# Performance work log

Measured on AMD Instinct MI355X. Metric: run time of the kernel, lower is better.

The kernel has to match this reference:

```python
import jax, jax.numpy as jnp
import numpy as np

B, Q, K, D, H, HD, OUT = 4, 1024, 1024, 256, 8, 32, 256


def setup_inputs() -> dict:
    key = jax.random.key(0)
    ks = jax.random.split(key, 11)
    s = 0.05  # small init scale for weights
    return {
        "q_data": jax.random.normal(ks[0], (B, Q, D), jnp.float32),
        "m_data": jax.random.normal(ks[1], (B, K, D), jnp.float32),
        "bias": jax.random.normal(ks[2], (B, 1, 1, K), jnp.float32),
        "nonbatched_bias": jax.random.normal(ks[3], (H, Q, K), jnp.float32),
        "query_w": jax.random.normal(ks[4], (D, H, HD), jnp.float32) * s,
        "key_w": jax.random.normal(ks[5], (D, H, HD), jnp.float32) * s,
        "value_w": jax.random.normal(ks[6], (D, H, HD), jnp.float32) * s,
        "gating_w": jax.random.normal(ks[7], (D, H, HD), jnp.float32) * s,
        "gating_b": jnp.ones((H, HD), jnp.float32),
        "output_w": jax.random.normal(ks[8], (H, HD, OUT), jnp.float32) * s,
        "output_b": jnp.zeros((OUT,), jnp.float32),
    }


def reference(q_data, m_data, bias, nonbatched_bias, query_w, key_w, value_w,
              gating_w, gating_b, output_w, output_b):
    key_dim = query_w.shape[-1]
    # QKV projections; queries pre-scaled by 1/sqrt(head_dim)
    q = jnp.einsum('bqa,ahc->bqhc', q_data, query_w) * key_dim ** (-0.5)
    k = jnp.einsum('bka,ahc->bkhc', m_data, key_w)
    v = jnp.einsum('bka,ahc->bkhc', m_data, value_w)
    # attention logits [b,h,q,k] plus batched and nonbatched additive biases
    logits_update = jnp.einsum('bqhc,bkhc->bhqk', q, k)
    logits = logits_update + bias + nonbatched_bias[None]
    weights = jax.nn.softmax(logits, axis=-1)
    weighted_avg = jnp.einsum('bhqk,bkhc->bqhc', weights, v)
    # sigmoid gating on the value-aggregated output
    gate = jax.nn.sigmoid(jnp.einsum('bqc,chv->bqhv', q_data, gating_w) + gating_b)
    weighted_avg = weighted_avg * gate
    output = jnp.einsum('bqhc,hco->bqo', weighted_avg, output_w) + output_b
    return (output, logits_update)
```

## Files before the change

kernel.cpp:

```cpp
#include <hip/hip_runtime.h>
#include <hip/hip_bf16.h>

#define NB 4
#define NQ 1024
#define NKS 1024
#define ND 256
#define NH 8
#define NHD 32
#define NOUT 256
#define SPLIT 4

typedef __attribute__((ext_vector_type(8))) short v8s;
typedef __attribute__((ext_vector_type(4))) short v4s;
typedef __attribute__((ext_vector_type(4))) float f32x4;

__global__ __launch_bounds__(256) void prep_all(
    const float* __restrict__ qd, const float* __restrict__ md,
    const float* __restrict__ qw, const float* __restrict__ kw,
    const float* __restrict__ vw, const float* __restrict__ gw,
    const float* __restrict__ ow,
    __hip_bfloat16* __restrict__ Abf, __hip_bfloat16* __restrict__ Wt)
{
  if (blockIdx.x < 1024) {
    const int gid = blockIdx.x * 256 + threadIdx.x;
    const float* src = (gid < 131072) ? qd : md;
    const size_t off = (size_t)(gid & 131071) * 8;
    const float4 a = ((const float4*)(src + off))[0];
    const float4 c = ((const float4*)(src + off))[1];
    __hip_bfloat16 t8[8];
    t8[0]=__float2bfloat16(a.x); t8[1]=__float2bfloat16(a.y);
    t8[2]=__float2bfloat16(a.z); t8[3]=__float2bfloat16(a.w);
    t8[4]=__float2bfloat16(c.x); t8[5]=__float2bfloat16(c.y);
    t8[6]=__float2bfloat16(c.z); t8[7]=__float2bfloat16(c.w);
    *(v8s*)(Abf + (size_t)gid * 8) = *(v8s*)t8;
    return;
  }
  __shared__ float tile[64][65];
  const int wb = blockIdx.x - 1024;
  const int m = wb >> 4, bx = wb & 15;
  const float* src = (m == 0) ? qw : (m == 1) ? kw : (m == 2) ? vw
                   : (m == 3) ? gw : ow;
  const float scale = (m == 0) ? 0.1767766952966369f : 1.0f;
  const int d0 = (bx >> 2) * 64, o0 = (bx & 3) * 64;
  #pragma unroll
  for (int i = 0; i < 16; ++i) {
    const int idx = threadIdx.x + i * 256;
    tile[idx >> 6][idx & 63] = src[(size_t)(d0 + (idx >> 6)) * 256 + o0 + (idx & 63)];
  }
  __syncthreads();
  __hip_bfloat16* dst = Wt + (size_t)m * 65536;
  #pragma unroll
  for (int i = 0; i < 16; ++i) {
    const int idx = threadIdx.x + i * 256;
    const int orow = idx >> 6, dc = idx & 63;
    dst[(size_t)(o0 + orow) * 256 + d0 + dc] = __float2bfloat16(tile[dc][orow] * scale);
  }
}

__global__ __launch_bounds__(256) void proj_kernel(
    const __hip_bfloat16* __restrict__ Abf, const __hip_bfloat16* __restrict__ Wt,
    const float* __restrict__ gating_b,
    __hip_bfloat16* __restrict__ Qw, __hip_bfloat16* __restrict__ Kw,
    __hip_bfloat16* __restrict__ Vt, __hip_bfloat16* __restrict__ G)
{
  const int wv = threadIdx.x >> 6, lane = threadIdx.x & 63;
  const int c = lane & 15, g = lane >> 4;
  const int task = blockIdx.x * 4 + wv;
  const int ctg = task & 3;
  const int mat = (task >> 2) & 1;
  const int r0g = (task >> 3) & 255;
  const int src = task >> 11;
  const int r0 = r0g * 16;
  const int b = r0 >> 10, pos0 = r0 & 1023;
  const f32x4 z = {0.f, 0.f, 0.f, 0.f};

  const __hip_bfloat16* A = Abf + ((size_t)src * 4096 + r0) * 256;
  v8s af[8];
  #pragma unroll
  for (int ks = 0; ks < 8; ++ks)
    af[ks] = *(const v8s*)(A + c * 256 + ks * 32 + g * 8);

  const int widx = (src == 0) ? (mat ? 3 : 0) : (mat ? 2 : 1);
  const __hip_bfloat16* W = Wt + (size_t)widx * 65536;
  const bool swapped = (src == 1) && (mat == 1);

  f32x4 ac[4] = {z, z, z, z};
  #pragma unroll
  for (int ks = 0; ks < 8; ++ks) {
    #pragma unroll
    for (int j = 0; j < 4; ++j) {
      v8s wf = *(const v8s*)(W + (size_t)((ctg * 4 + j) * 16 + c) * 256 + ks * 32 + g * 8);
      ac[j] = swapped
        ? __builtin_amdgcn_mfma_f32_16x16x32_bf16(wf, af[ks], ac[j], 0, 0, 0)
        : __builtin_amdgcn_mfma_f32_16x16x32_bf16(af[ks], wf, ac[j], 0, 0, 0);
    }
  }

  if (src == 0 && mat == 0) {
    #pragma unroll
    for (int j = 0; j < 4; ++j) {
      const int o = (ctg * 4 + j) * 16 + c, h = o >> 5, hd = o & 31;
      #pragma unroll
      for (int r = 0; r < 4; ++r)
        Qw[((size_t)(b * NH + h) * 1024 + pos0 + 4 * g + r) * 32 + hd] =
            __float2bfloat16(ac[j][r]);
    }
  } else if (src == 0) {
    #pragma unroll
    for (int j = 0; j < 4; ++j) {
      const int o = (ctg * 4 + j) * 16 + c;
      const float gb = gating_b[o];
      #pragma unroll
      for (int r = 0; r < 4; ++r)
        G[(size_t)(r0 + 4 * g + r) * 256 + o] = __float2bfloat16(ac[j][r] + gb);
    }
  } else if (mat == 0) {
    #pragma unroll
    for (int j = 0; j < 4; ++j) {
      const int o = (ctg * 4 + j) * 16 + c, h = o >> 5, hd = o & 31;
      #pragma unroll
      for (int r = 0; r < 4; ++r)
        Kw[((size_t)(b * NH + h) * 1024 + pos0 + 4 * g + r) * 32 + hd] =
            __float2bfloat16(ac[j][r]);
    }
  } else {
    #pragma unroll
    for (int j = 0; j < 4; ++j) {
      #pragma unroll
      for (int r = 0; r < 4; ++r) {
        const int o2 = (ctg * 4 + j) * 16 + 4 * g + r;
        Vt[((size_t)(b * NH + (o2 >> 5)) * 32 + (o2 & 31)) * 1024 + pos0 + c] =
            __float2bfloat16(ac[j][r]);
      }
    }
  }
}

__global__ __launch_bounds__(256, 2) void attn_kernel(
    const __hip_bfloat16* __restrict__ Qw, const __hip_bfloat16* __restrict__ Kw,
    const __hip_bfloat16* __restrict__ Vt,
    const float* __restrict__ bias, const float* __restrict__ nbb,
    float* __restrict__ out_logits,
    __hip_bfloat16* __restrict__ partO, float* __restrict__ partL)
{
  __shared__ __align__(16) __hip_bfloat16 sP[4][16][72];

  const int wv = threadIdx.x >> 6, lane = threadIdx.x & 63;
  const int c = lane & 15, g = lane >> 4;
  const int xcd   = blockIdx.x & 7;
  const int slot  = blockIdx.x >> 3;
  const int bh    = ((slot >> 6) << 3) | xcd;
  const int inner = slot & 63;
  const int sp    = inner >> 4;
  const int qtg   = inner & 15;
  const int qt  = qtg * 4 + wv;
  const int b = bh >> 3, h = bh & 7;
  const int rem = bh * 64 + qt;
  const int q0 = qt * 16;
  const int kbase = sp * (NKS / SPLIT);
  const size_t bhs = (size_t)bh;

  const __hip_bfloat16* Kbase = Kw + bhs * NKS * NHD;
  const __hip_bfloat16* Vbase = Vt + bhs * NHD * NKS;
  const float* biasb = bias + (size_t)b * NKS;
  const float* nbbb  = nbb + ((size_t)h * NQ + q0) * NKS;

  const v8s qfrag = *(const v8s*)(Qw + (bhs * NQ + q0 + c) * NHD + g * 8);

  const f32x4 zacc = {0.f, 0.f, 0.f, 0.f};
  f32x4 O0 = zacc, O1 = zacc;
  float lsumL[4] = {0.f, 0.f, 0.f, 0.f};

  auto loadKV = [&](int k0, v8s* kf, v8s* vf) {
    kf[0] = *(const v8s*)(Kbase + (k0 +      c) * NHD + g * 8);
    kf[1] = *(const v8s*)(Kbase + (k0 + 16 + c) * NHD + g * 8);
    kf[2] = *(const v8s*)(Kbase + (k0 + 32 + c) * NHD + g * 8);
    kf[3] = *(const v8s*)(Kbase + (k0 + 48 + c) * NHD + g * 8);
    vf[0] = *(const v8s*)(Vbase + (     c) * NKS + k0 +      g * 8);
    vf[1] = *(const v8s*)(Vbase + (16 + c) * NKS + k0 +      g * 8);
    vf[2] = *(const v8s*)(Vbase + (     c) * NKS + k0 + 32 + g * 8);
    vf[3] = *(const v8s*)(Vbase + (16 + c) * NKS + k0 + 32 + g * 8);
  };
  auto loadBias = [&](int k0, float* bn) {
    #pragma unroll
    for (int t = 0; t < 4; ++t) {
      const float bvt = biasb[k0 + t * 16 + c];
      #pragma unroll
      for (int r = 0; r < 4; ++r)
        bn[t * 4 + r] = bvt + nbbb[(g * 4 + r) * NKS + k0 + t * 16 + c];
    }
  };

  auto compute = [&](int k0, const v8s* kf, const v8s* vf, const float* bn) {
    f32x4 S[4];
    #pragma unroll
    for (int t = 0; t < 4; ++t)
      S[t] = __builtin_amdgcn_mfma_f32_16x16x32_bf16(qfrag, kf[t], zacc, 0, 0, 0);

    #pragma unroll
    for (int r = 0; r < 4; ++r) {
      const int qrow = q0 + g * 4 + r;
      float* lp = out_logits + (bhs * NQ + qrow) * (size_t)NKS + k0 + c;
      float psum = 0.f;
      #pragma unroll
      for (int t = 0; t < 4; ++t) {
        lp[t * 16] = S[t][r];
        const float p = __expf(S[t][r] + bn[t * 4 + r]);
        psum += p;
        sP[wv][g * 4 + r][t * 16 + c] = __float2bfloat16(p);
      }
      lsumL[r] += psum;
    }

    const v8s pa0 = *(const v8s*)&sP[wv][c][g * 8];
    const v8s pa1 = *(const v8s*)&sP[wv][c][32 + g * 8];
    O0 = __builtin_amdgcn_mfma_f32_16x16x32_bf16(pa0, vf[0], O0, 0, 0, 0);
    O0 = __builtin_amdgcn_mfma_f32_16x16x32_bf16(pa1, vf[2], O0, 0, 0, 0);
    O1 = __builtin_amdgcn_mfma_f32_16x16x32_bf16(pa0, vf[1], O1, 0, 0, 0);
    O1 = __builtin_amdgcn_mfma_f32_16x16x32_bf16(pa1, vf[3], O1, 0, 0, 0);
  };

  v8s kfA[4], vfA[4], kfB[4], vfB[4];
  float bnA[16], bnB[16];

  loadKV(kbase, kfA, vfA);
  loadBias(kbase, bnA);
  #pragma unroll 1
  for (int kt = 0; kt < NKS / SPLIT / 64; kt += 2) {
    loadKV(kbase + (kt + 1) * 64, kfB, vfB);
    loadBias(kbase + (kt + 1) * 64, bnB);
    compute(kbase + kt * 64, kfA, vfA, bnA);
    if (kt + 2 < NKS / SPLIT / 64) {
      loadKV(kbase + (kt + 2) * 64, kfA, vfA);
      loadBias(kbase + (kt + 2) * 64, bnA);
    }
    compute(kbase + (kt + 1) * 64, kfB, vfB, bnB);
  }

  #pragma unroll
  for (int r = 0; r < 4; ++r) {
    float rs = lsumL[r];
    rs += __shfl_xor(rs, 1);
    rs += __shfl_xor(rs, 2);
    rs += __shfl_xor(rs, 4);
    rs += __shfl_xor(rs, 8);
    const int row = 4 * g + r;
    const size_t pb = ((size_t)(rem * SPLIT + sp) * 16 + row) * 32;
    partO[pb + c]      = __float2bfloat16(O0[r]);
    partO[pb + 16 + c] = __float2bfloat16(O1[r]);
    if (c == 0) partL[(size_t)(rem * SPLIT + sp) * 16 + row] = rs;
  }
}

__global__ __launch_bounds__(256) void outproj_kernel(
    const __hip_bfloat16* __restrict__ partO, const float* __restrict__ partL,
    const __hip_bfloat16* __restrict__ G, const __hip_bfloat16* __restrict__ WtO,
    const float* __restrict__ output_b, float* __restrict__ out)
{
  __shared__ __align__(16) __hip_bfloat16 sRows[16][264];
  const int t = threadIdx.x;
  const int wv = t >> 6, lane = t & 63;
  const int c = lane & 15, g = lane >> 4;
  const int r0 = blockIdx.x * 16;
  const int b = r0 >> 10, qt = (r0 & 1023) >> 4;
  const int h = t >> 5, hd = t & 31;
  const int rem = (b * NH + h) * 64 + qt;

  #pragma unroll 4
  for (int row = 0; row < 16; ++row) {
    float o = 0.f, l = 0.f;
    #pragma unroll
    for (int sp = 0; sp < SPLIT; ++sp) {
      const size_t base = (size_t)(rem * SPLIT + sp) * 16 + row;
      o += __bfloat162float(partO[base * 32 + hd]);
      l += partL[base];
    }
    const float gl = __bfloat162float(G[(size_t)(r0 + row) * 256 + t]);
    sRows[row][t] = __float2bfloat16((o / l) * (1.f / (1.f + __expf(-gl))));
  }
  __syncthreads();

  const f32x4 z = {0.f, 0.f, 0.f, 0.f};
  f32x4 ac[4] = {z, z, z, z};
  #pragma unroll
  for (int ks = 0; ks < 8; ++ks) {
    const v8s af = *(const v8s*)&sRows[c][ks * 32 + g * 8];
    #pragma unroll
    for (int j = 0; j < 4; ++j) {
      const v8s wf = *(const v8s*)(WtO + (size_t)((wv * 4 + j) * 16 + c) * 256 + ks * 32 + g * 8);
      ac[j] = __builtin_amdgcn_mfma_f32_16x16x32_bf16(af, wf, ac[j], 0, 0, 0);
    }
  }
  #pragma unroll
  for (int j = 0; j < 4; ++j) {
    const int o = (wv * 4 + j) * 16 + c;
    const float ob = output_b[o];
    #pragma unroll
    for (int r = 0; r < 4; ++r)
      out[(size_t)(r0 + 4 * g + r) * 256 + o] = ac[j][r] + ob;
  }
}

extern "C" void kernel_launch(void* const* d_in, const int* in_sizes, int n_in,
                              void* d_out, int out_size, void* d_ws, size_t ws_size,
                              hipStream_t stream) {
  const float* q_data   = (const float*)d_in[0];
  const float* m_data   = (const float*)d_in[1];
  const float* bias     = (const float*)d_in[2];
  const float* nbb      = (const float*)d_in[3];
  const float* query_w  = (const float*)d_in[4];
  const float* key_w    = (const float*)d_in[5];
  const float* value_w  = (const float*)d_in[6];
  const float* gating_w = (const float*)d_in[7];
  const float* gating_b = (const float*)d_in[8];
  const float* output_w = (const float*)d_in[9];
  const float* output_b = (const float*)d_in[10];

  float* out        = (float*)d_out;
  float* out_logits = out + (size_t)NB * NQ * NOUT;

  char* ws = (char*)d_ws;
  const size_t MB = 1u << 20;
  __hip_bfloat16* Qw  = (__hip_bfloat16*)(ws);
  __hip_bfloat16* Kw  = (__hip_bfloat16*)(ws + 2 * MB);
  __hip_bfloat16* Vt  = (__hip_bfloat16*)(ws + 4 * MB);
  __hip_bfloat16* G   = (__hip_bfloat16*)(ws + 6 * MB);
  __hip_bfloat16* Abf = (__hip_bfloat16*)(ws + 10 * MB);
  __hip_bfloat16* partO = (__hip_bfloat16*)(ws + 10 * MB);
  float*          partL = (float*)(ws + 19 * MB);
  __hip_bfloat16* Wt  = (__hip_bfloat16*)(ws + 20 * MB);

  prep_all<<<1104, 256, 0, stream>>>(q_data, m_data, query_w, key_w, value_w,
                                     gating_w, output_w, Abf, Wt);
  proj_kernel<<<1024, 256, 0, stream>>>(Abf, Wt, gating_b, Qw, Kw, Vt, G);
  attn_kernel<<<2048, 256, 0, stream>>>(Qw, Kw, Vt, bias, nbb, out_logits, partO, partL);
  outproj_kernel<<<256, 256, 0, stream>>>(partO, partL, G, Wt + (size_t)4 * 65536,
                                          output_b, out);
}
```

Measured before the change: 84.73 us.

## Fuse input bf16 conversion into projection and shrink attention blocks to two waves

Removes the separate fp32-to-bf16 conversion pass over q_data and m_data. The projection kernel now reads fp32 inputs directly and converts them in registers, which cuts a write and re-read of an 8MB intermediate. The attention kernel moves from 256-thread blocks of 4 waves to 128-thread blocks of 2 waves with twice the grid, and the block-to-(bh, split, qtile) mapping is remapped to match. Each projection task now reads fp32 rows, twice the bytes of the old bf16 rows, and these may be re-read across the tasks that share a row. The attention launch bounds also drop the min-blocks hint.

Measured after the change: 85.98 us. No clear change (+1.5%).

```diff
diff --git a/kernel.cpp b/kernel.cpp
--- a/kernel.cpp
+++ b/kernel.cpp
@@ -14,29 +14,13 @@
 typedef __attribute__((ext_vector_type(4))) short v4s;
 typedef __attribute__((ext_vector_type(4))) float f32x4;
 
-__global__ __launch_bounds__(256) void prep_all(
-    const float* __restrict__ qd, const float* __restrict__ md,
+__global__ __launch_bounds__(256) void prep_w(
     const float* __restrict__ qw, const float* __restrict__ kw,
     const float* __restrict__ vw, const float* __restrict__ gw,
-    const float* __restrict__ ow,
-    __hip_bfloat16* __restrict__ Abf, __hip_bfloat16* __restrict__ Wt)
+    const float* __restrict__ ow, __hip_bfloat16* __restrict__ Wt)
 {
-  if (blockIdx.x < 1024) {
-    const int gid = blockIdx.x * 256 + threadIdx.x;
-    const float* src = (gid < 131072) ? qd : md;
-    const size_t off = (size_t)(gid & 131071) * 8;
-    const float4 a = ((const float4*)(src + off))[0];
-    const float4 c = ((const float4*)(src + off))[1];
-    __hip_bfloat16 t8[8];
-    t8[0]=__float2bfloat16(a.x); t8[1]=__float2bfloat16(a.y);
-    t8[2]=__float2bfloat16(a.z); t8[3]=__float2bfloat16(a.w);
-    t8[4]=__float2bfloat16(c.x); t8[5]=__float2bfloat16(c.y);
-    t8[6]=__float2bfloat16(c.z); t8[7]=__float2bfloat16(c.w);
-    *(v8s*)(Abf + (size_t)gid * 8) = *(v8s*)t8;
-    return;
-  }
   __shared__ float tile[64][65];
-  const int wb = blockIdx.x - 1024;
+  const int wb = blockIdx.x;
   const int m = wb >> 4, bx = wb & 15;
   const float* src = (m == 0) ? qw : (m == 1) ? kw : (m == 2) ? vw
                    : (m == 3) ? gw : ow;
@@ -58,8 +42,8 @@
 }
 
 __global__ __launch_bounds__(256) void proj_kernel(
-    const __hip_bfloat16* __restrict__ Abf, const __hip_bfloat16* __restrict__ Wt,
-    const float* __restrict__ gating_b,
+    const float* __restrict__ qdata, const float* __restrict__ mdata,
+    const __hip_bfloat16* __restrict__ Wt, const float* __restrict__ gating_b,
     __hip_bfloat16* __restrict__ Qw, __hip_bfloat16* __restrict__ Kw,
     __hip_bfloat16* __restrict__ Vt, __hip_bfloat16* __restrict__ G)
 {
@@ -74,11 +58,19 @@
   const int b = r0 >> 10, pos0 = r0 & 1023;
   const f32x4 z = {0.f, 0.f, 0.f, 0.f};
 
-  const __hip_bfloat16* A = Abf + ((size_t)src * 4096 + r0) * 256;
+  const float* A = (src ? mdata : qdata) + (size_t)(r0 + c) * 256;
   v8s af[8];
   #pragma unroll
-  for (int ks = 0; ks < 8; ++ks)
-    af[ks] = *(const v8s*)(A + c * 256 + ks * 32 + g * 8);
+  for (int ks = 0; ks < 8; ++ks) {
+    const f32x4 a0 = *(const f32x4*)(A + ks * 32 + g * 8);
+    const f32x4 a1 = *(const f32x4*)(A + ks * 32 + g * 8 + 4);
+    __hip_bfloat16 t8[8];
+    t8[0]=__float2bfloat16(a0.x); t8[1]=__float2bfloat16(a0.y);
+    t8[2]=__float2bfloat16(a0.z); t8[3]=__float2bfloat16(a0.w);
+    t8[4]=__float2bfloat16(a1.x); t8[5]=__float2bfloat16(a1.y);
+    t8[6]=__float2bfloat16(a1.z); t8[7]=__float2bfloat16(a1.w);
+    af[ks] = *(v8s*)t8;
+  }
 
   const int widx = (src == 0) ? (mat ? 3 : 0) : (mat ? 2 : 1);
   const __hip_bfloat16* W = Wt + (size_t)widx * 65536;
@@ -136,24 +128,24 @@
   }
 }
 
-__global__ __launch_bounds__(256, 2) void attn_kernel(
+__global__ __launch_bounds__(128) void attn_kernel(
     const __hip_bfloat16* __restrict__ Qw, const __hip_bfloat16* __restrict__ Kw,
     const __hip_bfloat16* __restrict__ Vt,
     const float* __restrict__ bias, const float* __restrict__ nbb,
     float* __restrict__ out_logits,
     __hip_bfloat16* __restrict__ partO, float* __restrict__ partL)
 {
-  __shared__ __align__(16) __hip_bfloat16 sP[4][16][72];
+  __shared__ __align__(16) __hip_bfloat16 sP[2][16][72];
 
   const int wv = threadIdx.x >> 6, lane = threadIdx.x & 63;
   const int c = lane & 15, g = lane >> 4;
   const int xcd   = blockIdx.x & 7;
   const int slot  = blockIdx.x >> 3;
-  const int bh    = ((slot >> 6) << 3) | xcd;
-  const int inner = slot & 63;
-  const int sp    = inner >> 4;
-  const int qtg   = inner & 15;
-  const int qt  = qtg * 4 + wv;
+  const int bh    = ((slot >> 7) << 3) | xcd;
+  const int inner = slot & 127;
+  const int sp    = inner >> 5;
+  const int qtg   = inner & 31;
+  const int qt  = qtg * 2 + wv;
   const int b = bh >> 3, h = bh & 7;
   const int rem = bh * 64 + qt;
   const int q0 = qt * 16;
@@ -325,15 +317,13 @@
   __hip_bfloat16* Kw  = (__hip_bfloat16*)(ws + 2 * MB);
   __hip_bfloat16* Vt  = (__hip_bfloat16*)(ws + 4 * MB);
   __hip_bfloat16* G   = (__hip_bfloat16*)(ws + 6 * MB);
-  __hip_bfloat16* Abf = (__hip_bfloat16*)(ws + 10 * MB);
   __hip_bfloat16* partO = (__hip_bfloat16*)(ws + 10 * MB);
   float*          partL = (float*)(ws + 19 * MB);
   __hip_bfloat16* Wt  = (__hip_bfloat16*)(ws + 20 * MB);
 
-  prep_all<<<1104, 256, 0, stream>>>(q_data, m_data, query_w, key_w, value_w,
-                                     gating_w, output_w, Abf, Wt);
-  proj_kernel<<<1024, 256, 0, stream>>>(Abf, Wt, gating_b, Qw, Kw, Vt, G);
-  attn_kernel<<<2048, 256, 0, stream>>>(Qw, Kw, Vt, bias, nbb, out_logits, partO, partL);
+  prep_w<<<80, 256, 0, stream>>>(query_w, key_w, value_w, gating_w, output_w, Wt);
+  proj_kernel<<<1024, 256, 0, stream>>>(q_data, m_data, Wt, gating_b, Qw, Kw, Vt, G);
+  attn_kernel<<<4096, 128, 0, stream>>>(Qw, Kw, Vt, bias, nbb, out_logits, partO, partL);
   outproj_kernel<<<256, 256, 0, stream>>>(partO, partL, G, Wt + (size_t)4 * 65536,
                                           output_b, out);
 }
```
